# Kernel optimization log

Hardware: AMD Instinct MI355X
Metric: run time of the kernel (lower is better)

The kernel has to match this reference:

```python
import jax, jax.numpy as jnp
import numpy as np

BATCH, SEQ_LEN, NUM_TAGS = 1024, 512, 48


def setup_inputs() -> dict:
    key = jax.random.key(0)
    k1, k2 = jax.random.split(key)
    potentials = jax.random.normal(k1, (BATCH, SEQ_LEN, NUM_TAGS), dtype=jnp.float32)
    transition_params = jax.random.normal(k2, (NUM_TAGS, NUM_TAGS), dtype=jnp.float32)
    return {"potentials": potentials, "transition_params": transition_params}


def reference(potentials, transition_params):
    """Viterbi forward decode for a linear-chain CRF.

    potentials: [B, T, num_tags] unary potentials.
    transition_params: [num_tags, num_tags] binary potentials.
    Returns:
      backpointers: [B, T-1, num_tags] int32 argmax backpointers.
      scores: [B, num_tags] final Viterbi scores.
    """
    init_state = potentials[:, 0]                 # [B, num_tags]
    rest = jnp.swapaxes(potentials[:, 1:], 0, 1)  # [T-1, B, num_tags]

    def step(state, inputs):
        # state: [B, num_tags]; inputs: [B, num_tags]
        # transition_scores[b, i, j] = state[b, i] + trans[i, j]
        transition_scores = state[:, :, None] + transition_params[None]  # [B, tags, tags]
        new_state = inputs + jnp.max(transition_scores, axis=1)          # [B, tags]
        backpointers = jnp.argmax(transition_scores, axis=1).astype(jnp.int32)
        return new_state, backpointers

    final_state, backpointers = jax.lax.scan(step, init_state, rest)
    backpointers = jnp.swapaxes(backpointers, 0, 1)  # [B, T-1, num_tags]
    return backpointers, final_state
```

## Files before the change

kernel.cpp:

```cpp
#include <hip/hip_runtime.h>


constexpr int B_ = 1024;
constexpr int T_ = 512;
constexpr int K_ = 48;
constexpr int C_ = 6;

__global__ __launch_bounds__(64, 1) void crf_viterbi_kernel(
    const float* __restrict__ pot,
    const float* __restrict__ trans,
    float* __restrict__ out)
{
    const int b = blockIdx.x;
    const int j = threadIdx.x;

    __shared__ __align__(16) float stv[K_];

    float tcol[K_];
    #pragma unroll
    for (int i = 0; i < K_; ++i) tcol[i] = trans[i * K_ + j];

    const float* pp = pot + (size_t)b * T_ * K_ + j;
    float* bpp      = out + (size_t)b * (T_ - 1) * K_ + j;
    float* scout    = out + (size_t)B_ * (T_ - 1) * K_ + (size_t)b * K_ + j;

    float myst = pp[0];
    stv[j] = myst;
    __builtin_amdgcn_wave_barrier();

    float candA[K_], candB[K_];
    float mmA = 0.0f, mmB = 0.0f;

    float bpf0 = 0.0f, bpf1 = 0.0f, bpf2 = 0.0f,
          bpf3 = 0.0f, bpf4 = 0.0f, bpf5 = 0.0f;

#define STEP(PCUR, CN, CO, MMN, MMO, DOSH, BPV)                                \
    do {                                                                       \
         \
        float4 sv[12];                                                         \
        const float4* stv4 = (const float4*)stv;                               \
        _Pragma("unroll")                                                      \
        for (int c = 0; c < 12; ++c) sv[c] = stv4[c];                          \
         \
        if (DOSH) {                                                            \
            int xx = K_ - 1;                                                   \
            _Pragma("unroll")                                                  \
            for (int i = K_ - 2; i >= 0; --i)                                  \
                xx = (CO[i] == MMO) ? i : xx;            \
            BPV = (float)xx;                                                   \
            *bpp = BPV;                                                        \
            bpp += K_;                                                         \
        }                                                                      \
              \
        _Pragma("unroll")                                                      \
        for (int c = 0; c < 12; ++c) {                                         \
            CN[4 * c + 0] = sv[c].x + tcol[4 * c + 0];                         \
            CN[4 * c + 1] = sv[c].y + tcol[4 * c + 1];                         \
            CN[4 * c + 2] = sv[c].z + tcol[4 * c + 2];                         \
            CN[4 * c + 3] = sv[c].w + tcol[4 * c + 3];                         \
        }                                                                      \
         \
        float m1[16];                                                          \
        _Pragma("unroll")                                                      \
        for (int k = 0; k < 16; ++k)                                           \
            m1[k] = fmaxf(fmaxf(CN[3 * k], CN[3 * k + 1]), CN[3 * k + 2]);     \
        float m2[6];                                                           \
        _Pragma("unroll")                                                      \
        for (int k = 0; k < 5; ++k)                                            \
            m2[k] = fmaxf(fmaxf(m1[3 * k], m1[3 * k + 1]), m1[3 * k + 2]);     \
        m2[5] = m1[15];                                                        \
        float m30 = fmaxf(fmaxf(m2[0], m2[1]), m2[2]);                         \
        float m31 = fmaxf(fmaxf(m2[3], m2[4]), m2[5]);                         \
        float mm  = fmaxf(m30, m31);                                           \
        MMN = mm;                                                              \
           \
        myst = (PCUR) + mm;                                                    \
        stv[j] = myst;                                                         \
        __builtin_amdgcn_wave_barrier();                                       \
    } while (0)

    float p1 = pp[(size_t)1 * K_];
    float pbuf[C_];
    #pragma unroll
    for (int u = 0; u < C_; ++u) pbuf[u] = pp[(size_t)(2 + u) * K_];

    STEP(p1, candB, candA, mmB, mmA, false, bpf0);

    for (int t0 = 2; t0 < T_; t0 += C_) {
        float pc[C_];
        #pragma unroll
        for (int u = 0; u < C_; ++u) pc[u] = pbuf[u];

        #pragma unroll
        for (int u = 0; u < C_; ++u) {
            int tn = t0 + C_ + u;
            if (tn > T_ - 1) tn = T_ - 1;
            pbuf[u] = pp[(size_t)tn * K_];
        }

        STEP(pc[0], candA, candB, mmA, mmB, true, bpf0);
        STEP(pc[1], candB, candA, mmB, mmA, true, bpf1);
        STEP(pc[2], candA, candB, mmA, mmB, true, bpf2);
        STEP(pc[3], candB, candA, mmB, mmA, true, bpf3);
        STEP(pc[4], candA, candB, mmA, mmB, true, bpf4);
        STEP(pc[5], candB, candA, mmB, mmA, true, bpf5);
    }

    {
        int xx = K_ - 1;
        #pragma unroll
        for (int i = K_ - 2; i >= 0; --i)
            xx = (candB[i] == mmB) ? i : xx;
        *bpp = (float)xx;
    }

    asm volatile("" :: "v"(bpf0), "v"(bpf1), "v"(bpf2),
                       "v"(bpf3), "v"(bpf4), "v"(bpf5));

    *scout = myst;
#undef STEP
}

extern "C" void kernel_launch(void* const* d_in, const int* in_sizes, int n_in,
                              void* d_out, int out_size, void* d_ws, size_t ws_size,
                              hipStream_t stream) {
    const float* pot   = (const float*)d_in[0];
    const float* trans = (const float*)d_in[1];
    float* out         = (float*)d_out;
    crf_viterbi_kernel<<<dim3(B_), dim3(K_), 0, stream>>>(pot, trans, out);
}
```

Measured before the change: 313.7 us.

## Split Viterbi max over four waves with readlane broadcast and LDS combine

Each batch element now gets a 256-thread block of four waves, and each wave handles 12 of the 48 source states. Each wave takes the state vector straight from registers with readlane broadcasts, instead of reading it from LDS. It computes a partial max and lowest-index argmax, writes the pair to a double-buffered LDS array, and all four waves merge after a block barrier, keeping the lower index on ties. This shortens the per-step serial max/argmax chain and raises waves per CU. The cost is a __syncthreads and extra LDS traffic on every time step.

```diff
diff --git a/kernel.cpp b/kernel.cpp
--- a/kernel.cpp
+++ b/kernel.cpp
@@ -5,78 +5,99 @@
 constexpr int T_ = 512;
 constexpr int K_ = 48;
 constexpr int C_ = 6;
+constexpr int NW_ = 4;
+constexpr int IS_ = 12;
 
-__global__ __launch_bounds__(64, 1) void crf_viterbi_kernel(
+__global__ __launch_bounds__(256, 4) void crf_viterbi_kernel(
     const float* __restrict__ pot,
     const float* __restrict__ trans,
     float* __restrict__ out)
 {
-    const int b = blockIdx.x;
-    const int j = threadIdx.x;
+    const int b    = blockIdx.x;
+    const int tid  = threadIdx.x;
+    const int w    = tid >> 6;
+    const int lane = tid & 63;
+    const int j    = (lane < K_) ? lane : (K_ - 1);
+    const bool st_ok = (lane < K_);
+    const int IB   = w * IS_;
 
-    __shared__ __align__(16) float stv[K_];
+    __shared__ float2 part[2][NW_][K_];
 
-    float tcol[K_];
+    float tcol[IS_];
     #pragma unroll
-    for (int i = 0; i < K_; ++i) tcol[i] = trans[i * K_ + j];
+    for (int k = 0; k < IS_; ++k) tcol[k] = trans[(IB + k) * K_ + j];
+
+    float idxf[IS_];
+    #pragma unroll
+    for (int k = 0; k < IS_; ++k) idxf[k] = (float)(IB + k);
+    const float BIGF = 256.0f;
 
     const float* pp = pot + (size_t)b * T_ * K_ + j;
     float* bpp      = out + (size_t)b * (T_ - 1) * K_ + j;
     float* scout    = out + (size_t)B_ * (T_ - 1) * K_ + (size_t)b * K_ + j;
 
     float myst = pp[0];
-    stv[j] = myst;
-    __builtin_amdgcn_wave_barrier();
-
-    float candA[K_], candB[K_];
-    float mmA = 0.0f, mmB = 0.0f;
+    float st[IS_];
+    #pragma unroll
+    for (int k = 0; k < IS_; ++k)
+        st[k] = __int_as_float(
+            __builtin_amdgcn_readlane(__float_as_int(myst), IB + k));
 
     float bpf0 = 0.0f, bpf1 = 0.0f, bpf2 = 0.0f,
           bpf3 = 0.0f, bpf4 = 0.0f, bpf5 = 0.0f;
 
-#define STEP(PCUR, CN, CO, MMN, MMO, DOSH, BPV)                                \
+#define STEP(PCUR, PAR, BPV)                                                   \
     do {                                                                       \
-         \
-        float4 sv[12];                                                         \
-        const float4* stv4 = (const float4*)stv;                               \
+        float cand[IS_];                                                       \
         _Pragma("unroll")                                                      \
-        for (int c = 0; c < 12; ++c) sv[c] = stv4[c];                          \
-         \
-        if (DOSH) {                                                            \
-            int xx = K_ - 1;                                                   \
-            _Pragma("unroll")                                                  \
-            for (int i = K_ - 2; i >= 0; --i)                                  \
-                xx = (CO[i] == MMO) ? i : xx;            \
-            BPV = (float)xx;                                                   \
-            *bpp = BPV;                                                        \
-            bpp += K_;                                                         \
-        }                                                                      \
-              \
+        for (int k = 0; k < IS_; ++k) cand[k] = st[k] + tcol[k];               \
+                              \
+        float a0 = fmaxf(fmaxf(cand[0], cand[1]),  cand[2]);                   \
+        float a1 = fmaxf(fmaxf(cand[3], cand[4]),  cand[5]);                   \
+        float a2 = fmaxf(fmaxf(cand[6], cand[7]),  cand[8]);                   \
+        float a3 = fmaxf(fmaxf(cand[9], cand[10]), cand[11]);                  \
+        float pm = fmaxf(fmaxf(a0, a1), fmaxf(a2, a3));                        \
+                  \
+        float e0  = (cand[0]  == pm) ? idxf[0]  : BIGF;                        \
+        float e1  = (cand[1]  == pm) ? idxf[1]  : BIGF;                        \
+        float e2  = (cand[2]  == pm) ? idxf[2]  : BIGF;                        \
+        float e3  = (cand[3]  == pm) ? idxf[3]  : BIGF;                        \
+        float e4  = (cand[4]  == pm) ? idxf[4]  : BIGF;                        \
+        float e5  = (cand[5]  == pm) ? idxf[5]  : BIGF;                        \
+        float e6  = (cand[6]  == pm) ? idxf[6]  : BIGF;                        \
+        float e7  = (cand[7]  == pm) ? idxf[7]  : BIGF;                        \
+        float e8  = (cand[8]  == pm) ? idxf[8]  : BIGF;                        \
+        float e9  = (cand[9]  == pm) ? idxf[9]  : BIGF;                        \
+        float e10 = (cand[10] == pm) ? idxf[10] : BIGF;                        \
+        float e11 = (cand[11] == pm) ? idxf[11] : BIGF;                        \
+        float f0 = fminf(fminf(e0, e1),  e2);                                  \
+        float f1 = fminf(fminf(e3, e4),  e5);                                  \
+        float f2 = fminf(fminf(e6, e7),  e8);                                  \
+        float f3 = fminf(fminf(e9, e10), e11);                                 \
+        float af = fminf(fminf(f0, f1), fminf(f2, f3));                        \
+        part[PAR][w][j] = make_float2(pm, af);                                 \
+        __syncthreads();                                                       \
+        float2 q0 = part[PAR][0][j];                                           \
+        float2 q1 = part[PAR][1][j];                                           \
+        float2 q2 = part[PAR][2][j];                                           \
+        float2 q3 = part[PAR][3][j];                                           \
+          \
+        bool c01 = (q1.x > q0.x);                                              \
+        float bm01 = c01 ? q1.x : q0.x;                                        \
+        float bp01 = c01 ? q1.y : q0.y;                                        \
+        bool c23 = (q3.x > q2.x);                                              \
+        float bm23 = c23 ? q3.x : q2.x;                                        \
+        float bp23 = c23 ? q3.y : q2.y;                                        \
+        bool cw = (bm23 > bm01);                                               \
+        float bm = cw ? bm23 : bm01;                                           \
+        BPV = cw ? bp23 : bp01;                                                \
+        if (w == 0 && st_ok) *bpp = BPV;                       \
+        bpp += K_;                                                             \
+        myst = (PCUR) + bm;                                                    \
         _Pragma("unroll")                                                      \
-        for (int c = 0; c < 12; ++c) {                                         \
-            CN[4 * c + 0] = sv[c].x + tcol[4 * c + 0];                         \
-            CN[4 * c + 1] = sv[c].y + tcol[4 * c + 1];                         \
-            CN[4 * c + 2] = sv[c].z + tcol[4 * c + 2];                         \
-            CN[4 * c + 3] = sv[c].w + tcol[4 * c + 3];                         \
-        }                                                                      \
-         \
-        float m1[16];                                                          \
-        _Pragma("unroll")                                                      \
-        for (int k = 0; k < 16; ++k)                                           \
-            m1[k] = fmaxf(fmaxf(CN[3 * k], CN[3 * k + 1]), CN[3 * k + 2]);     \
-        float m2[6];                                                           \
-        _Pragma("unroll")                                                      \
-        for (int k = 0; k < 5; ++k)                                            \
-            m2[k] = fmaxf(fmaxf(m1[3 * k], m1[3 * k + 1]), m1[3 * k + 2]);     \
-        m2[5] = m1[15];                                                        \
-        float m30 = fmaxf(fmaxf(m2[0], m2[1]), m2[2]);                         \
-        float m31 = fmaxf(fmaxf(m2[3], m2[4]), m2[5]);                         \
-        float mm  = fmaxf(m30, m31);                                           \
-        MMN = mm;                                                              \
-           \
-        myst = (PCUR) + mm;                                                    \
-        stv[j] = myst;                                                         \
-        __builtin_amdgcn_wave_barrier();                                       \
+        for (int k = 0; k < IS_; ++k)                                          \
+            st[k] = __int_as_float(                                            \
+                __builtin_amdgcn_readlane(__float_as_int(myst), IB + k));      \
     } while (0)
 
     float p1 = pp[(size_t)1 * K_];
@@ -84,7 +105,7 @@
     #pragma unroll
     for (int u = 0; u < C_; ++u) pbuf[u] = pp[(size_t)(2 + u) * K_];
 
-    STEP(p1, candB, candA, mmB, mmA, false, bpf0);
+    STEP(p1, 1, bpf5);
 
     for (int t0 = 2; t0 < T_; t0 += C_) {
         float pc[C_];
@@ -98,26 +119,18 @@
             pbuf[u] = pp[(size_t)tn * K_];
         }
 
-        STEP(pc[0], candA, candB, mmA, mmB, true, bpf0);
-        STEP(pc[1], candB, candA, mmB, mmA, true, bpf1);
-        STEP(pc[2], candA, candB, mmA, mmB, true, bpf2);
-        STEP(pc[3], candB, candA, mmB, mmA, true, bpf3);
-        STEP(pc[4], candA, candB, mmA, mmB, true, bpf4);
-        STEP(pc[5], candB, candA, mmB, mmA, true, bpf5);
-    }
-
-    {
-        int xx = K_ - 1;
-        #pragma unroll
-        for (int i = K_ - 2; i >= 0; --i)
-            xx = (candB[i] == mmB) ? i : xx;
-        *bpp = (float)xx;
+        STEP(pc[0], 0, bpf0);
+        STEP(pc[1], 1, bpf1);
+        STEP(pc[2], 0, bpf2);
+        STEP(pc[3], 1, bpf3);
+        STEP(pc[4], 0, bpf4);
+        STEP(pc[5], 1, bpf5);
     }
 
     asm volatile("" :: "v"(bpf0), "v"(bpf1), "v"(bpf2),
                        "v"(bpf3), "v"(bpf4), "v"(bpf5));
 
-    *scout = myst;
+    if (w == 0 && st_ok) *scout = myst;
 #undef STEP
 }
 
@@ -127,5 +140,5 @@
     const float* pot   = (const float*)d_in[0];
     const float* trans = (const float*)d_in[1];
     float* out         = (float*)d_out;
-    crf_viterbi_kernel<<<dim3(B_), dim3(K_), 0, stream>>>(pot, trans, out);
+    crf_viterbi_kernel<<<dim3(B_), dim3(256), 0, stream>>>(pot, trans, out);
 }
```

Result: slower. 513.8 us (+63.8%).
